# Optimization experiments

Measured on AMD Instinct MI355X. Metric: run time of the kernel, lower is better.

## Reference

```python
import jax, jax.numpy as jnp
import numpy as np
from jax import lax

DN = ('NHWC', 'HWIO', 'NHWC')

def _conv(x, w):
    return lax.conv_general_dilated(x, w, window_strides=(1, 1), padding='SAME', dimension_numbers=DN)

def _hard_sigmoid(z):
    # keras hard_sigmoid: clip(0.2*z + 0.5, 0, 1) -- default recurrent_activation of ConvLSTM2D
    return jnp.clip(0.2 * z + 0.5, 0.0, 1.0)

def setup_inputs() -> dict:
    key = jax.random.key(0)
    ks = jax.random.split(key, 6)
    B, T, H, W, Cin = 4, 16, 64, 64, 32
    F, kh, kw = 64, 3, 3
    x  = jax.random.normal(ks[0], (B, T, H, W, Cin), dtype=jnp.float32)
    Wx = jax.random.normal(ks[1], (kh, kw, Cin, 4 * F), dtype=jnp.float32) * 0.05
    Wh = jax.random.normal(ks[2], (kh, kw, F, 4 * F), dtype=jnp.float32) * 0.05
    b  = jnp.zeros((4 * F,), dtype=jnp.float32)
    Wp = jax.random.normal(ks[3], (1, 1, Cin, F), dtype=jnp.float32) * 0.05
    bp = jnp.zeros((F,), dtype=jnp.float32)
    return {"x": x, "Wx": Wx, "Wh": Wh, "b": b, "Wp": Wp, "bp": bp}

def reference(x, Wx, Wh, b, Wp, bp):
    B, T, H, W, Cin = x.shape
    F = Wh.shape[2]
    # Precompute the input-to-gate convolutions for all timesteps at once.
    zx = _conv(x.reshape(B * T, H, W, Cin), Wx) + b          # (B*T, H, W, 4F)
    zx = zx.reshape(B, T, H, W, 4 * F).transpose(1, 0, 2, 3, 4)  # time-major

    def step(carry, zx_t):
        h, c = carry
        z = zx_t + _conv(h, Wh)                              # (B, H, W, 4F)
        zi, zf, zc, zo = jnp.split(z, 4, axis=-1)            # keras gate order i,f,c,o
        i = _hard_sigmoid(zi)
        f = _hard_sigmoid(zf)
        c_new = f * c + i * jnp.tanh(zc)
        o = _hard_sigmoid(zo)
        h_new = o * jnp.tanh(c_new)
        return (h_new, c_new), h_new

    h0 = jnp.zeros((B, H, W, F), dtype=x.dtype)
    c0 = jnp.zeros((B, H, W, F), dtype=x.dtype)
    _, hs = lax.scan(step, (h0, c0), zx)                     # (T, B, H, W, F)
    convlstm_out = hs.transpose(1, 0, 2, 3, 4)               # (B, T, H, W, F)

    # TimeDistributed 1x1 projection of the input as the residual branch.
    residual = _conv(x.reshape(B * T, H, W, Cin), Wp) + bp
    residual = residual.reshape(B, T, H, W, F)
    return convlstm_out + residual
```

## Files before the change

kernel.cpp:

```cpp
#include <hip/hip_runtime.h>

#define B_ 4
#define T_ 16
#define H_ 64
#define W_ 64
#define CIN 32
#define F_ 64
#define NCH 256
#define KSTEPS 27
#define NPHASE 14
#define WSTEP 10240
#define PHSTEP 20480
#define TSLAB (H_ * W_ * F_)

#define OFF_H0 589824
#define OFF_H1 2686976

typedef __attribute__((ext_vector_type(8))) short short8;
typedef __attribute__((ext_vector_type(4))) float floatx4;
typedef __attribute__((address_space(3))) unsigned int  lds_u32;
typedef __attribute__((address_space(1))) const unsigned int g_u32;

__device__ __forceinline__ unsigned short f2bf(float f) {
  union { float f; unsigned u; } v; v.f = f;
  unsigned r = v.u + 0x7FFFu + ((v.u >> 16) & 1u);
  return (unsigned short)(r >> 16);
}

__device__ __forceinline__ float tanh_fast(float z) {
  float e = __expf(2.0f * z);
  return 1.0f - 2.0f * __builtin_amdgcn_rcpf(e + 1.0f);
}

__global__ void prep_weights(const float* __restrict__ Wx, const float* __restrict__ Wh,
                             unsigned short* __restrict__ WT) {
  int idx = blockIdx.x * 256 + threadIdx.x;
  int s = idx / WSTEP;
  int r = idx - s * WSTEP;
  int n = r / 40;
  int c = r - n * 40;
  unsigned short v = 0;
  if (c < 32 && s < KSTEPS) {
    int k  = s * 32 + c;
    int g  = k / 96;
    int ch = k - g * 96;
    float f = (ch < CIN) ? Wx[(g * CIN + ch) * NCH + n]
                         : Wh[(g * F_ + (ch - CIN)) * NCH + n];
    v = f2bf(f);
  }
  WT[idx] = v;
}

__global__ void prep_zero_h(float4* __restrict__ p) {
  int idx = blockIdx.x * 256 + threadIdx.x;
  p[idx] = make_float4(0.f, 0.f, 0.f, 0.f);
}

__global__ void prep_zero_c(float* __restrict__ out) {
  int idx = blockIdx.x * 256 + threadIdx.x;
  int b = idx >> 16;
  int i = idx & 65535;
  ((float4*)(out + (size_t)b * (T_ * TSLAB)))[i] = make_float4(0.f, 0.f, 0.f, 0.f);
}

__device__ __forceinline__ void stage_wt2(const unsigned short* __restrict__ src,
                                          short* dstbuf, int w, int lane) {
  __attribute__((address_space(3))) unsigned short* d =
      (__attribute__((address_space(3))) unsigned short*)dstbuf;
  const unsigned short* s = src + lane * 8;
  __builtin_amdgcn_global_load_lds((g_u32*)(s + w * 512),
                                   (lds_u32*)(d + w * 512), 16, 0, 0);
  __builtin_amdgcn_global_load_lds((g_u32*)(s + (w + 16) * 512),
                                   (lds_u32*)(d + (w + 16) * 512), 16, 0, 0);
  if (w < 8)
    __builtin_amdgcn_global_load_lds((g_u32*)(s + (w + 32) * 512),
                                     (lds_u32*)(d + (w + 32) * 512), 16, 0, 0);
}

__global__ __launch_bounds__(1024, 1)
void step_kernel(const float* __restrict__ x, const float* __restrict__ bias,
                 const float* __restrict__ Wp, const float* __restrict__ bp,
                 const unsigned short* __restrict__ WT,
                 const unsigned short* __restrict__ hprev,
                 unsigned short* __restrict__ hnew,
                 float* __restrict__ out, int t)
{
  __shared__ __align__(16) char smem[110208];
  short* patch = (short*)smem;
  short* bl0   = (short*)(smem + 28288);
  short* bl1   = (short*)(smem + 69248);
  float* gact  = (float*)smem;
  float* WpL   = (float*)(smem + 69632);

  const int tid  = threadIdx.x;
  const int w    = tid >> 6;
  const int lane = tid & 63;
  const int quad = lane >> 4;
  const int lr   = lane & 15;
  const int gate = w >> 2;
  const int mq   = w & 3;

  const int raw = blockIdx.x;
  const int bid = (raw & 7) * 32 + (raw >> 3);
  const int b   = bid >> 6;
  const int rem = bid & 63;
  const int y0  = (rem >> 1) << 1;
  const int x0  = (rem & 1) << 5;

  stage_wt2(WT, bl0, w, lane);

  if (tid < 272) {
    int e = tid >> 1, half = tid & 1;
    int sy = e / 34, sx = e - sy * 34;
    int yy = y0 + sy - 1, xx = x0 + sx - 1;
    short* dst = patch + e * 104;
    bool in = (yy >= 0 && yy < H_ && xx >= 0 && xx < W_);
    if (half == 0) {
      if (in) {
        const float4* xs = (const float4*)(x + ((((b * T_ + t) * H_ + yy) * W_ + xx) * CIN));
        #pragma unroll
        for (int j = 0; j < 4; j++) {
          float4 f0 = xs[2 * j];
          float4 f1 = xs[2 * j + 1];
          union { short8 v; unsigned short u[8]; } pk;
          pk.u[0] = f2bf(f0.x); pk.u[1] = f2bf(f0.y); pk.u[2] = f2bf(f0.z); pk.u[3] = f2bf(f0.w);
          pk.u[4] = f2bf(f1.x); pk.u[5] = f2bf(f1.y); pk.u[6] = f2bf(f1.z); pk.u[7] = f2bf(f1.w);
          ((short8*)dst)[j] = pk.v;
        }
      } else {
        uint4 z = make_uint4(0, 0, 0, 0);
        uint4* d4 = (uint4*)dst;
        #pragma unroll
        for (int j = 0; j < 4; j++) d4[j] = z;
      }
    } else {
      uint4* d2 = (uint4*)(dst + 32);
      if (in) {
        const uint4* hs = (const uint4*)(hprev + ((b * H_ + yy) * W_ + xx) * F_);
        #pragma unroll
        for (int j = 0; j < 8; j++) d2[j] = hs[j];
      } else {
        uint4 z = make_uint4(0, 0, 0, 0);
        #pragma unroll
        for (int j = 0; j < 8; j++) d2[j] = z;
      }
    }
  }

  float bias_r[4];
  #pragma unroll
  for (int nf = 0; nf < 4; nf++) bias_r[nf] = bias[gate * 64 + nf * 16 + lr];

  floatx4 acc[4];
  #pragma unroll
  for (int nf = 0; nf < 4; nf++) acc[nf] = (floatx4){0.f, 0.f, 0.f, 0.f};

  const int px = mq * 16 + lr;
  const int ty = px >> 5, tx = px & 31;

  __syncthreads();

  const unsigned short* wsrc = WT + PHSTEP;
  for (int p = 0; p < NPHASE; p++) {
    short* cur = (p & 1) ? bl1 : bl0;
    if (p < NPHASE - 1) {
      stage_wt2(wsrc, (p & 1) ? bl0 : bl1, w, lane);
      wsrc += PHSTEP;
    }
    #pragma unroll
    for (int half = 0; half < 2; half++) {
      int s = 2 * p + half;
      if (s < KSTEPS) {
        int g  = s / 3;
        int c0 = (s - g * 3) * 32;
        int dy = g / 3, dx = g - dy * 3;
        short8 afr = *(const short8*)(patch + ((ty + dy) * 34 + tx + dx) * 104 + c0 + quad * 8);
        #pragma unroll
        for (int nf = 0; nf < 4; nf++) {
          short8 bfr = *(const short8*)(cur + half * WSTEP + (gate * 64 + nf * 16 + lr) * 40 + quad * 8);
          acc[nf] = __builtin_amdgcn_mfma_f32_16x16x32_bf16(afr, bfr, acc[nf], 0, 0, 0);
        }
      }
    }
    __syncthreads();
  }

  #pragma unroll
  for (int nf = 0; nf < 4; nf++)
    #pragma unroll
    for (int r = 0; r < 4; r++) {
      int mm = quad * 4 + r;
      float z = acc[nf][r] + bias_r[nf];
      float a;
      if (gate == 2) a = tanh_fast(z);
      else {
        a = __builtin_fmaf(z, 0.2f, 0.5f);
        a = fminf(fmaxf(a, 0.f), 1.f);
      }
      gact[(gate * 64 + mq * 16 + mm) * 68 + nf * 16 + lr] = a;
    }
  if (tid < 512)
    ((float4*)WpL)[tid] = ((const float4*)Wp)[tid];

  const int mloc = tid >> 4;
  const int cb   = (tid & 15) * 4;
  const int tyo  = mloc >> 5, txo = mloc & 31;
  const int gy   = y0 + tyo, gx = x0 + txo;
  const int hbase   = ((b * H_ + gy) * W_ + gx) * F_ + cb;
  const int outbase = (((b * T_ + t) * H_ + gy) * W_ + gx) * F_ + cb;

  float xv[32];
  {
    const float4* xs = (const float4*)(x + ((((b * T_ + t) * H_ + gy) * W_ + gx) * CIN));
    #pragma unroll
    for (int j = 0; j < 8; j++) {
      float4 f = xs[j];
      xv[4 * j] = f.x; xv[4 * j + 1] = f.y; xv[4 * j + 2] = f.z; xv[4 * j + 3] = f.w;
    }
  }
  float4 co4 = *(const float4*)(out + outbase);

  __syncthreads();

  float res[4];
  #pragma unroll
  for (int j = 0; j < 4; j++) res[j] = bp[cb + j];
  #pragma unroll
  for (int ci = 0; ci < 32; ci++) {
    float xf = xv[ci];
    float4 wv = *(const float4*)(WpL + ci * 64 + cb);
    res[0] += xf * wv.x; res[1] += xf * wv.y; res[2] += xf * wv.z; res[3] += xf * wv.w;
  }

  float4 gi = *(const float4*)(gact + (0 * 64 + mloc) * 68 + cb);
  float4 gf = *(const float4*)(gact + (1 * 64 + mloc) * 68 + cb);
  float4 gg = *(const float4*)(gact + (2 * 64 + mloc) * 68 + cb);
  float4 go = *(const float4*)(gact + (3 * 64 + mloc) * 68 + cb);
  float cold[4] = {co4.x, co4.y, co4.z, co4.w};
  float iv[4] = {gi.x, gi.y, gi.z, gi.w};
  float fv[4] = {gf.x, gf.y, gf.z, gf.w};
  float gv[4] = {gg.x, gg.y, gg.z, gg.w};
  float ov[4] = {go.x, go.y, go.z, go.w};
  float cn4[4], h4[4];
  union { unsigned short hv[4]; uint2 q; } hu;
  #pragma unroll
  for (int e = 0; e < 4; e++) {
    float cn = fv[e] * cold[e] + iv[e] * gv[e];
    float h  = ov[e] * tanh_fast(cn);
    cn4[e] = cn; h4[e] = h;
    hu.hv[e] = f2bf(h);
  }
  if (t < T_ - 1)
    *(float4*)(out + outbase + TSLAB) = make_float4(cn4[0], cn4[1], cn4[2], cn4[3]);
  *(float4*)(out + outbase) = make_float4(h4[0] + res[0], h4[1] + res[1],
                                          h4[2] + res[2], h4[3] + res[3]);
  *(uint2*)(hnew + hbase) = hu.q;
}

extern "C" void kernel_launch(void* const* d_in, const int* in_sizes, int n_in,
                              void* d_out, int out_size, void* d_ws, size_t ws_size,
                              hipStream_t stream) {
  const float* x    = (const float*)d_in[0];
  const float* Wx   = (const float*)d_in[1];
  const float* Wh   = (const float*)d_in[2];
  const float* bias = (const float*)d_in[3];
  const float* Wp   = (const float*)d_in[4];
  const float* bp   = (const float*)d_in[5];
  float* out = (float*)d_out;

  unsigned short* WT = (unsigned short*)d_ws;
  unsigned short* h0 = (unsigned short*)((char*)d_ws + OFF_H0);
  unsigned short* h1 = (unsigned short*)((char*)d_ws + OFF_H1);

  hipLaunchKernelGGL(prep_weights, dim3(1120), dim3(256), 0, stream, Wx, Wh, WT);
  hipLaunchKernelGGL(prep_zero_h, dim3(1024), dim3(256), 0, stream,
                     (float4*)((char*)d_ws + OFF_H0));
  hipLaunchKernelGGL(prep_zero_c, dim3(1024), dim3(256), 0, stream, out);

  for (int t = 0; t < T_; t++) {
    const unsigned short* hp = (t & 1) ? h1 : h0;
    unsigned short*       hn = (t & 1) ? h0 : h1;
    hipLaunchKernelGGL(step_kernel, dim3(256), dim3(1024), 0, stream,
                       x, bias, Wp, bp, WT, hp, hn, out, t);
  }
}
```

Before: 656.1 us.

## Triple-buffer weight staging with fine-grained vmcnt waits instead of full syncs

The weight-phase staging moves from a double to a triple LDS buffer, so loads for phase p+2 are issued while phase p computes. The full __syncthreads after each phase becomes a partial s_waitcnt vmcnt that waits only for the older phase's loads, followed by s_barrier. Load distribution across waves is also rebalanced so each wave issues a fixed count (3 or 2), which makes the vmcnt thresholds exact. LDS usage grows to about 151KB, which still fits with one block per CU but leaves less headroom.

Measured after the change: 680.4 us. 1.04x slower.

```diff
diff --git a/kernel.cpp b/kernel.cpp
--- a/kernel.cpp
+++ b/kernel.cpp
@@ -10,7 +10,7 @@
 #define KSTEPS 27
 #define NPHASE 14
 #define WSTEP 10240
-#define PHSTEP 20480
+#define PHS   20480
 #define TSLAB (H_ * W_ * F_)
 
 #define OFF_H0 589824
@@ -63,18 +63,26 @@
   ((float4*)(out + (size_t)b * (T_ * TSLAB)))[i] = make_float4(0.f, 0.f, 0.f, 0.f);
 }
 
-__device__ __forceinline__ void stage_wt2(const unsigned short* __restrict__ src,
-                                          short* dstbuf, int w, int lane) {
+__device__ __forceinline__ void stage_ph(const unsigned short* __restrict__ src,
+                                         short* dstbuf, int w, int lane) {
   __attribute__((address_space(3))) unsigned short* d =
       (__attribute__((address_space(3))) unsigned short*)dstbuf;
   const unsigned short* s = src + lane * 8;
-  __builtin_amdgcn_global_load_lds((g_u32*)(s + w * 512),
-                                   (lds_u32*)(d + w * 512), 16, 0, 0);
-  __builtin_amdgcn_global_load_lds((g_u32*)(s + (w + 16) * 512),
-                                   (lds_u32*)(d + (w + 16) * 512), 16, 0, 0);
-  if (w < 8)
-    __builtin_amdgcn_global_load_lds((g_u32*)(s + (w + 32) * 512),
-                                     (lds_u32*)(d + (w + 32) * 512), 16, 0, 0);
+  if (w < 8) {
+    #pragma unroll
+    for (int i = 0; i < 3; i++) {
+      int q = w * 3 + i;
+      __builtin_amdgcn_global_load_lds((g_u32*)(s + q * 512),
+                                       (lds_u32*)(d + q * 512), 16, 0, 0);
+    }
+  } else {
+    #pragma unroll
+    for (int i = 0; i < 2; i++) {
+      int q = 24 + (w - 8) * 2 + i;
+      __builtin_amdgcn_global_load_lds((g_u32*)(s + q * 512),
+                                       (lds_u32*)(d + q * 512), 16, 0, 0);
+    }
+  }
 }
 
 __global__ __launch_bounds__(1024, 1)
@@ -85,10 +93,11 @@
                  unsigned short* __restrict__ hnew,
                  float* __restrict__ out, int t)
 {
-  __shared__ __align__(16) char smem[110208];
+  __shared__ __align__(16) char smem[151168];
   short* patch = (short*)smem;
-  short* bl0   = (short*)(smem + 28288);
-  short* bl1   = (short*)(smem + 69248);
+  short* wb0   = (short*)(smem + 28288);
+  short* wb1   = (short*)(smem + 69248);
+  short* wb2   = (short*)(smem + 110208);
   float* gact  = (float*)smem;
   float* WpL   = (float*)(smem + 69632);
 
@@ -107,7 +116,7 @@
   const int y0  = (rem >> 1) << 1;
   const int x0  = (rem & 1) << 5;
 
-  stage_wt2(WT, bl0, w, lane);
+  stage_ph(WT, wb0, w, lane);
 
   if (tid < 272) {
     int e = tid >> 1, half = tid & 1;
@@ -147,6 +156,8 @@
     }
   }
 
+  stage_ph(WT + PHS, wb1, w, lane);
+
   float bias_r[4];
   #pragma unroll
   for (int nf = 0; nf < 4; nf++) bias_r[nf] = bias[gate * 64 + nf * 16 + lr];
@@ -158,18 +169,24 @@
   const int px = mq * 16 + lr;
   const int ty = px >> 5, tx = px & 31;
 
-  __syncthreads();
-
-  const unsigned short* wsrc = WT + PHSTEP;
+  asm volatile("s_waitcnt vmcnt(0) lgkmcnt(0)" ::: "memory");
+  __builtin_amdgcn_sched_barrier(0);
+  __builtin_amdgcn_s_barrier();
+  __builtin_amdgcn_sched_barrier(0);
+
+  short* b0 = wb0;
+  short* b1 = wb1;
+  short* b2 = wb2;
+  const unsigned short* wsrc = WT + 2 * PHS;
   for (int p = 0; p < NPHASE; p++) {
-    short* cur = (p & 1) ? bl1 : bl0;
-    if (p < NPHASE - 1) {
-      stage_wt2(wsrc, (p & 1) ? bl0 : bl1, w, lane);
-      wsrc += PHSTEP;
-    }
+    if (p < NPHASE - 2) {
+      stage_ph(wsrc, b2, w, lane);
+      wsrc += PHS;
+    }
+    int s0 = 2 * p;
     #pragma unroll
     for (int half = 0; half < 2; half++) {
-      int s = 2 * p + half;
+      int s = s0 + half;
       if (s < KSTEPS) {
         int g  = s / 3;
         int c0 = (s - g * 3) * 32;
@@ -177,12 +194,22 @@
         short8 afr = *(const short8*)(patch + ((ty + dy) * 34 + tx + dx) * 104 + c0 + quad * 8);
         #pragma unroll
         for (int nf = 0; nf < 4; nf++) {
-          short8 bfr = *(const short8*)(cur + half * WSTEP + (gate * 64 + nf * 16 + lr) * 40 + quad * 8);
+          short8 bfr = *(const short8*)(b0 + half * WSTEP + (gate * 64 + nf * 16 + lr) * 40 + quad * 8);
           acc[nf] = __builtin_amdgcn_mfma_f32_16x16x32_bf16(afr, bfr, acc[nf], 0, 0, 0);
         }
       }
     }
-    __syncthreads();
+    __builtin_amdgcn_sched_barrier(0);
+    if (p < NPHASE - 2) {
+      if (w < 8) asm volatile("s_waitcnt vmcnt(3)" ::: "memory");
+      else       asm volatile("s_waitcnt vmcnt(2)" ::: "memory");
+    } else {
+      asm volatile("s_waitcnt vmcnt(0)" ::: "memory");
+    }
+    __builtin_amdgcn_sched_barrier(0);
+    __builtin_amdgcn_s_barrier();
+    __builtin_amdgcn_sched_barrier(0);
+    { short* tmp = b0; b0 = b1; b1 = b2; b2 = tmp; }
   }
 
   #pragma unroll
```
